# Performance work log

Measured on AMD Instinct MI355X. Metric: run time of the kernel, lower is better.

## Reference

```python
import jax, jax.numpy as jnp
import numpy as np

N_HEAD = 12

def setup_inputs() -> dict:
    key = jax.random.key(0)
    k1, k2, k3 = jax.random.split(key, 3)
    B, T, C = 8, 1024, 768
    x = jax.random.normal(k1, (B, T, C), dtype=jnp.float32)
    # torch Linear(768, 3*768): store as [in, out] so we can do x @ W
    W_attn = jax.random.normal(k2, (C, 3 * C), dtype=jnp.float32) * 0.02
    b_attn = jax.random.normal(k3, (3 * C,), dtype=jnp.float32) * 0.02
    return {"x": x, "W_attn": W_attn, "b_attn": b_attn}

def reference(x, W_attn, b_attn):
    B, T, C = x.shape
    H = N_HEAD
    hs = C // H
    scale = 1.0 / jnp.sqrt(jnp.asarray(hs, dtype=x.dtype))
    qkv = x @ W_attn + b_attn                      # [B,T,3C]
    q, k, v = jnp.split(qkv, 3, axis=-1)
    q = q.reshape(B, T, H, hs).transpose(0, 2, 1, 3)  # [B,H,T,hs]
    k = k.reshape(B, T, H, hs).transpose(0, 2, 1, 3)
    v = v.reshape(B, T, H, hs).transpose(0, 2, 1, 3)
    scores = jnp.einsum('bhqd,bhkd->bhqk', q, k) * scale
    # causal mask then ReLU (masked -inf entries become 0 after ReLU)
    causal = jnp.tril(jnp.ones((T, T), dtype=bool))
    att = jnp.where(causal[None, None], jax.nn.relu(scores), jnp.zeros((), dtype=scores.dtype))
    out = jnp.einsum('bhqk,bhkd->bhqd', att, v)    # [B,H,T,hs]
    out = out.transpose(0, 2, 1, 3).reshape(B, T, C)
    return out
```

## Files before the change

### kernel.cpp

```cpp
#include <hip/hip_runtime.h>

typedef __attribute__((ext_vector_type(8))) short bf16x8;
typedef __attribute__((ext_vector_type(4))) float f32x4;
typedef __attribute__((ext_vector_type(4))) unsigned short us4;
typedef __attribute__((ext_vector_type(8))) unsigned short us8;

#define MFMA(a, b, c) __builtin_amdgcn_mfma_f32_16x16x32_bf16((a), (b), (c), 0, 0, 0)

__device__ __forceinline__ unsigned short f2bf(float f) {
  unsigned u = __builtin_bit_cast(unsigned, f);
  u = (u + 0x7fffu + ((u >> 16) & 1u)) >> 16;
  return (unsigned short)u;
}

__device__ __forceinline__ unsigned cvt_pk_bf16(float lo, float hi) {
  unsigned r;
  asm("v_cvt_pk_bf16_f32 %0, %1, %2" : "=v"(r) : "v"(lo), "v"(hi));
  return r;
}

__device__ __forceinline__ void gload16(const void* g, void* l) {
  __builtin_amdgcn_global_load_lds((const __attribute__((address_space(1))) void*)g,
                                   (__attribute__((address_space(3))) void*)l,
                                   16, 0, 0);
}

__device__ __forceinline__ bf16x8 readfrag(const unsigned short* buf, int row, int kbyte) {
  int byte = row * 128 + kbyte;
  byte ^= (row & 7) << 4;
  return *(const bf16x8*)((const char*)buf + byte);
}

__global__ void cast_x_kernel(const float* __restrict__ x,
                              unsigned short* __restrict__ xb, int n4) {
  int id = blockIdx.x * blockDim.x + threadIdx.x;
  if (id >= n4) return;
  float4 v = ((const float4*)x)[id];
  us4 o = { f2bf(v.x), f2bf(v.y), f2bf(v.z), f2bf(v.w) };
  ((us4*)xb)[id] = o;
}

__global__ void castw_kernel(const float* __restrict__ W,
                             unsigned short* __restrict__ Wt) {
  __shared__ unsigned short tile[32][33];
  int bn = blockIdx.x * 32;
  int bk = blockIdx.y * 32;
  int lx = threadIdx.x & 31, ly = threadIdx.x >> 5;
#pragma unroll
  for (int i = 0; i < 32; i += 8)
    tile[ly + i][lx] = f2bf(W[(bk + ly + i) * 2304 + bn + lx]);
  __syncthreads();
#pragma unroll
  for (int i = 0; i < 32; i += 8)
    Wt[(bn + ly + i) * 768 + bk + lx] = tile[lx][ly + i];
}

__global__ __launch_bounds__(256, 2) void qkv_gemm_kernel(
    const unsigned short* __restrict__ xb, const unsigned short* __restrict__ wt,
    const float* __restrict__ bias,
    unsigned short* __restrict__ qb, unsigned short* __restrict__ kb,
    unsigned short* __restrict__ vb) {
  __shared__ unsigned short lds[40960];
  const int tid = threadIdx.x;
  const int lane = tid & 63, wid = tid >> 6;
  const int wm = wid >> 1, wn = wid & 1;
  const int l15 = lane & 15, lg = lane >> 4;

  int bid = blockIdx.x;
  int xcd = bid & 7, c = bid >> 3;
  int mb = xcd * 8 + (c & 7);
  int nb = c >> 3;
  const int m0 = mb * 128, n0 = nb * 128;

  const unsigned short* Ab_g = xb + (size_t)m0 * 768;
  const unsigned short* Bb_g = wt + (size_t)n0 * 768;

  int eA[4], sA[4];
#pragma unroll
  for (int i = 0; i < 4; ++i) {
    int e = (i * 256 + tid) * 8, row = e >> 6;
    eA[i] = e;
    sA[i] = row * 768 + ((e ^ ((row & 7) << 3)) & 63);
  }

#define SA(buf, k0, i) gload16(Ab_g + sA[i] + (k0), &lds[(buf) * 8192 + eA[i]])
#define SB(buf, k0, i) gload16(Bb_g + sA[i] + (k0), &lds[24576 + (buf) * 8192 + eA[i]])

  f32x4 acc[4][4] = {};
  bf16x8 bfr[4][2];

  SA(0, 0, 0); SA(0, 0, 1); SA(0, 0, 2); SA(0, 0, 3);
  SB(0, 0, 0); SB(0, 0, 1); SB(0, 0, 2); SB(0, 0, 3);
  SA(1, 64, 0); SA(1, 64, 1); SA(1, 64, 2); SA(1, 64, 3);
  asm volatile("s_waitcnt vmcnt(4)" ::: "memory");
  __builtin_amdgcn_s_barrier();

#define GPHASE(cA_, cB_, P, STG, EW)                                              \
  {                                                                               \
    const unsigned short* Abuf = &lds[(cA_) * 8192];                              \
    const unsigned short* Bbuf = &lds[24576 + (cB_) * 8192];                      \
    bf16x8 afr[2][2];                                                             \
    _Pragma("unroll") for (int m2 = 0; m2 < 2; ++m2)                              \
        _Pragma("unroll") for (int kk = 0; kk < 2; ++kk)                          \
            afr[m2][kk] =                                                         \
        readfrag(Abuf, wm * 64 + ((P) * 2 + m2) * 16 + l15, kk * 64 + lg * 16);   \
    if ((P) == 0) {                                                               \
      _Pragma("unroll") for (int nf = 0; nf < 4; ++nf)                            \
          _Pragma("unroll") for (int kk = 0; kk < 2; ++kk)                        \
              bfr[nf][kk] =                                                       \
          readfrag(Bbuf, wn * 64 + nf * 16 + l15, kk * 64 + lg * 16);             \
    }                                                                             \
    STG;                                                                          \
    __builtin_amdgcn_sched_barrier(0);                                            \
    __builtin_amdgcn_s_barrier();                                                 \
    asm volatile("s_waitcnt lgkmcnt(0)" ::: "memory");                            \
    __builtin_amdgcn_sched_barrier(0);                                            \
    __builtin_amdgcn_s_setprio(1);                                                \
    _Pragma("unroll") for (int m2 = 0; m2 < 2; ++m2)                              \
        _Pragma("unroll") for (int nf = 0; nf < 4; ++nf)                          \
            _Pragma("unroll") for (int kk = 0; kk < 2; ++kk)                      \
                acc[(P) * 2 + m2][nf] =                                           \
        MFMA(afr[m2][kk], bfr[nf][kk], acc[(P) * 2 + m2][nf]);                    \
    __builtin_amdgcn_s_setprio(0);                                                \
    EW;                                                                           \
    __builtin_amdgcn_sched_barrier(0);                                            \
    __builtin_amdgcn_s_barrier();                                                 \
  }

  int cA = 0;
  for (int t = 0; t < 10; ++t) {
    int cB = t & 1, cBn = cB ^ 1;
    int cA2 = cA + 2; if (cA2 >= 3) cA2 -= 3;
    int k1 = (t + 1) * 64, k2 = (t + 2) * 64;
    GPHASE(cA, cB, 0, { SB(cBn, k1, 0); SB(cBn, k1, 1); SB(cBn, k1, 2); SB(cBn, k1, 3); }, );
    GPHASE(cA, cB, 1, { SA(cA2, k2, 0); SA(cA2, k2, 1); SA(cA2, k2, 2); SA(cA2, k2, 3); },
           asm volatile("s_waitcnt vmcnt(4)" ::: "memory"));
    cA = (cA == 2) ? 0 : cA + 1;
  }
  GPHASE(cA, 0, 0, { SB(1, 704, 0); SB(1, 704, 1); SB(1, 704, 2); SB(1, 704, 3); }, );
  GPHASE(cA, 0, 1, , asm volatile("s_waitcnt vmcnt(0)" ::: "memory"));
  cA = (cA == 2) ? 0 : cA + 1;
  GPHASE(cA, 1, 0, , );
  GPHASE(cA, 1, 1, , );

  __syncthreads();

  const int sec = n0 / 768;
  const float qs = (sec == 0) ? 0.125f : 1.0f;
  float bcol[4];
#pragma unroll
  for (int nf = 0; nf < 4; ++nf) bcol[nf] = bias[n0 + wn * 64 + nf * 16 + l15];

  if (sec < 2) {
    unsigned short* ct = lds;
#pragma unroll
    for (int mf = 0; mf < 4; ++mf)
#pragma unroll
      for (int nf = 0; nf < 4; ++nf)
#pragma unroll
        for (int r = 0; r < 4; ++r)
          ct[(wm * 64 + mf * 16 + lg * 4 + r) * 128 + wn * 64 + nf * 16 + l15] =
              f2bf((acc[mf][nf][r] + bcol[nf]) * qs);
    __syncthreads();
    unsigned short* dstbase = (sec == 0) ? qb : kb;
    const int hbase = (n0 - sec * 768) >> 6;
    const int g8 = tid >> 3, l8 = tid & 7;
#pragma unroll
    for (int j = 0; j < 8; ++j) {
      int chunk = j * 32 + g8;
      int row = chunk >> 1, hh = chunk & 1;
      us8 v = *(const us8*)&ct[row * 128 + hh * 64 + l8 * 8];
      int t = m0 + row, bb = t >> 10, tt = t & 1023;
      *(us8*)(dstbase + ((size_t)((bb * 12 + hbase + hh) * 1024 + tt)) * 64 + l8 * 8) = v;
    }
  } else {
#pragma unroll
    for (int nf = 0; nf < 4; ++nf) {
      int cc2 = (n0 - 1536) + wn * 64 + nf * 16 + l15;
      int h = cc2 >> 6, d = cc2 & 63;
#pragma unroll
      for (int mf = 0; mf < 4; ++mf) {
        int row0 = m0 + wm * 64 + mf * 16 + lg * 4;
        int bb = row0 >> 10, t0 = row0 & 1023;
        us4 o;
#pragma unroll
        for (int r = 0; r < 4; ++r) o[r] = f2bf(acc[mf][nf][r] + bcol[nf]);
        *(us4*)(vb + ((size_t)((bb * 12 + h) * 64 + d)) * 1024 + t0) = o;
      }
    }
  }
#undef SA
#undef SB
#undef GPHASE
}

__global__ __launch_bounds__(512, 2) void attn_kernel(
    const unsigned short* __restrict__ qb, const unsigned short* __restrict__ kb,
    const unsigned short* __restrict__ vb, float* __restrict__ out) {
  __shared__ unsigned short lds[65536];
  const int tid = threadIdx.x;
  const int lane = tid & 63, wid = tid >> 6;
  const int qs = wid >> 1, ks = wid & 1;
  const int l15 = lane & 15, lg = lane >> 4;

  int bid = blockIdx.x;
  int xcd = bid & 7, c = bid >> 3;
  int bh = xcd * 12 + (c % 12);
  int byq = 3 - (c / 12);
  const int b = bh / 12, h = bh % 12;
  const size_t base = (size_t)bh * 65536;
  const int Q = byq * 4 + qs;
  const int qr0 = byq * 256 + qs * 64;

  bf16x8 aq[4][2];
#pragma unroll
  for (int mf = 0; mf < 4; ++mf)
#pragma unroll
    for (int kk = 0; kk < 2; ++kk)
      aq[mf][kk] = *(const bf16x8*)(qb + base + (size_t)(qr0 + mf * 16 + l15) * 64 +
                                    kk * 32 + lg * 8);

  const int e = tid * 8;
  const int row = e >> 6;
  const int esw = e ^ ((row & 7) << 3);

#define ASTAGE(buf, i_)                                                            \
  {                                                                                \
    int kt0 = 2 * (i_);                                                            \
    gload16(kb + base + (size_t)kt0 * 4096 + esw, &lds[(buf) * 8192 + e]);         \
    gload16(kb + base + (size_t)(kt0 + 1) * 4096 + esw,                            \
            &lds[(buf) * 8192 + 4096 + e]);                                        \
    gload16(vb + base + (size_t)row * 1024 + kt0 * 64 + (esw & 63),                \
            &lds[16384 + (buf) * 8192 + e]);                                       \
    gload16(vb + base + (size_t)row * 1024 + (kt0 + 1) * 64 + (esw & 63),          \
            &lds[16384 + (buf) * 8192 + 4096 + e]);                                \
  }

  f32x4 o[4][4] = {};
  unsigned short* Sb = &lds[32768 + wid * 4096];

  const int niter = 2 * byq + 2;
  ASTAGE(0, 0);
  asm volatile("s_waitcnt vmcnt(0)" ::: "memory");
  __builtin_amdgcn_s_barrier();

  for (int i = 0; i < niter; ++i) {
    const int cur = i & 1;
    if (i + 1 < niter) ASTAGE(cur ^ 1, i + 1);
    const int kt = 2 * i + ks;
    if (kt <= Q) {
      const unsigned short* Kb = &lds[cur * 8192 + ks * 4096];
      const unsigned short* Vb = &lds[16384 + cur * 8192 + ks * 4096];
      bf16x8 bk[4][2];
#pragma unroll
      for (int nf = 0; nf < 4; ++nf)
#pragma unroll
        for (int kk = 0; kk < 2; ++kk)
          bk[nf][kk] = readfrag(Kb, nf * 16 + l15, kk * 64 + lg * 16);
      const bool diag = (kt == Q);
      __builtin_amdgcn_s_setprio(1);
#pragma unroll
      for (int mf = 0; mf < 4; ++mf)
#pragma unroll
        for (int nf = 0; nf < 4; ++nf) {
          f32x4 s = {};
          s = MFMA(bk[nf][0], aq[mf][0], s);
          s = MFMA(bk[nf][1], aq[mf][1], s);
          float v0, v1, v2, v3;
          if (diag) {
            int q = mf * 16 + l15, k0 = nf * 16 + lg * 4;
            v0 = (k0 + 0 <= q) ? fmaxf(s[0], 0.0f) : 0.0f;
            v1 = (k0 + 1 <= q) ? fmaxf(s[1], 0.0f) : 0.0f;
            v2 = (k0 + 2 <= q) ? fmaxf(s[2], 0.0f) : 0.0f;
            v3 = (k0 + 3 <= q) ? fmaxf(s[3], 0.0f) : 0.0f;
          } else {
            v0 = fmaxf(s[0], 0.0f);
            v1 = fmaxf(s[1], 0.0f);
            v2 = fmaxf(s[2], 0.0f);
            v3 = fmaxf(s[3], 0.0f);
          }
          uint2 w;
          w.x = cvt_pk_bf16(v0, v1);
          w.y = cvt_pk_bf16(v2, v3);
          int rowq = mf * 16 + l15;
          int byte = (rowq * 128 + (nf * 16 + lg * 4) * 2) ^ ((rowq & 7) << 4);
          *(uint2*)((char*)Sb + byte) = w;
        }
      __builtin_amdgcn_s_setprio(0);
      bf16x8 pa[4][2];
#pragma unroll
      for (int mf = 0; mf < 4; ++mf)
#pragma unroll
        for (int kk = 0; kk < 2; ++kk)
          pa[mf][kk] = readfrag(Sb, mf * 16 + l15, kk * 64 + lg * 16);
      __builtin_amdgcn_s_setprio(1);
#pragma unroll
      for (int mf = 0; mf < 4; ++mf)
#pragma unroll
        for (int df = 0; df < 4; ++df)
#pragma unroll
          for (int kk = 0; kk < 2; ++kk)
            o[mf][df] = MFMA(pa[mf][kk], readfrag(Vb, df * 16 + l15, kk * 64 + lg * 16),
                             o[mf][df]);
      __builtin_amdgcn_s_setprio(0);
    }
    asm volatile("s_waitcnt vmcnt(0)" ::: "memory");
    __builtin_amdgcn_sched_barrier(0);
    __builtin_amdgcn_s_barrier();
  }
#undef ASTAGE

  float* fr = (float*)lds;
  if (ks == 1) {
#pragma unroll
    for (int mf = 0; mf < 4; ++mf)
#pragma unroll
      for (int df = 0; df < 4; ++df)
#pragma unroll
        for (int r = 0; r < 4; ++r) {
          int rowq = mf * 16 + lg * 4 + r, col = df * 16 + l15;
          int idx = (qs * 4096 + rowq * 64 + col) ^ ((rowq & 4) << 2);
          fr[idx] = o[mf][df][r];
        }
  }
  __syncthreads();
  if (ks == 0) {
#pragma unroll
    for (int mf = 0; mf < 4; ++mf)
#pragma unroll
      for (int df = 0; df < 4; ++df)
#pragma unroll
        for (int r = 0; r < 4; ++r) {
          int rowq = mf * 16 + lg * 4 + r, col = df * 16 + l15;
          int idx = (qs * 4096 + rowq * 64 + col) ^ ((rowq & 4) << 2);
          float v = o[mf][df][r] + fr[idx];
          out[(size_t)(b * 1024 + qr0 + rowq) * 768 + h * 64 + col] = v;
        }
  }
}

extern "C" void kernel_launch(void* const* d_in, const int* in_sizes, int n_in,
                              void* d_out, int out_size, void* d_ws, size_t ws_size,
                              hipStream_t stream) {
  const float* x = (const float*)d_in[0];
  const float* W = (const float*)d_in[1];
  const float* bias = (const float*)d_in[2];
  float* out = (float*)d_out;

  unsigned short* xb = (unsigned short*)d_ws;
  unsigned short* wt = xb + 6291456;
  unsigned short* qb = wt + 1769472;
  unsigned short* kb = qb + 6291456;
  unsigned short* vb = kb + 6291456;

  cast_x_kernel<<<6144, 256, 0, stream>>>(x, xb, 1572864);
  castw_kernel<<<dim3(72, 24), 256, 0, stream>>>(W, wt);
  qkv_gemm_kernel<<<1152, 256, 0, stream>>>(xb, wt, bias, qb, kb, vb);
  attn_kernel<<<384, 512, 0, stream>>>(qb, kb, vb, out);
}
```

Baseline: 84.09 us.

## Keep P in registers via 16x16x16 MFMA and drop key-split waves

New measurement: 86.92 us. 3.4% more time.

```diff
diff --git a/kernel.cpp b/kernel.cpp
--- a/kernel.cpp
+++ b/kernel.cpp
@@ -1,11 +1,13 @@
 #include <hip/hip_runtime.h>
 
 typedef __attribute__((ext_vector_type(8))) short bf16x8;
+typedef __attribute__((ext_vector_type(4))) short bf16x4;
 typedef __attribute__((ext_vector_type(4))) float f32x4;
 typedef __attribute__((ext_vector_type(4))) unsigned short us4;
 typedef __attribute__((ext_vector_type(8))) unsigned short us8;
 
 #define MFMA(a, b, c) __builtin_amdgcn_mfma_f32_16x16x32_bf16((a), (b), (c), 0, 0, 0)
+#define MFMA16(a, b, c) __builtin_amdgcn_mfma_f32_16x16x16bf16_1k((a), (b), (c), 0, 0, 0)
 
 __device__ __forceinline__ unsigned short f2bf(float f) {
   unsigned u = __builtin_bit_cast(unsigned, f);
@@ -29,6 +31,11 @@
   int byte = row * 128 + kbyte;
   byte ^= (row & 7) << 4;
   return *(const bf16x8*)((const char*)buf + byte);
+}
+
+__device__ __forceinline__ bf16x4 readfrag64(const unsigned short* buf, int row, int col) {
+  int byte = (row * 128 + col * 2) ^ ((row & 7) << 4);
+  return *(const bf16x4*)((const char*)buf + byte);
 }
 
 __global__ void cast_x_kernel(const float* __restrict__ x,
@@ -146,7 +153,7 @@
   __syncthreads();
 
   const int sec = n0 / 768;
-  const float qs = (sec == 0) ? 0.125f : 1.0f;
+  const float qscale = (sec == 0) ? 0.125f : 1.0f;
   float bcol[4];
 #pragma unroll
   for (int nf = 0; nf < 4; ++nf) bcol[nf] = bias[n0 + wn * 64 + nf * 16 + l15];
@@ -160,7 +167,7 @@
 #pragma unroll
         for (int r = 0; r < 4; ++r)
           ct[(wm * 64 + mf * 16 + lg * 4 + r) * 128 + wn * 64 + nf * 16 + l15] =
-              f2bf((acc[mf][nf][r] + bcol[nf]) * qs);
+              f2bf((acc[mf][nf][r] + bcol[nf]) * qscale);
     __syncthreads();
     unsigned short* dstbase = (sec == 0) ? qb : kb;
     const int hbase = (n0 - sec * 768) >> 6;
@@ -194,13 +201,12 @@
 #undef GPHASE
 }
 
-__global__ __launch_bounds__(512, 2) void attn_kernel(
+__global__ __launch_bounds__(256, 2) void attn_kernel(
     const unsigned short* __restrict__ qb, const unsigned short* __restrict__ kb,
     const unsigned short* __restrict__ vb, float* __restrict__ out) {
-  __shared__ unsigned short lds[65536];
+  __shared__ unsigned short lds[16384];
   const int tid = threadIdx.x;
   const int lane = tid & 63, wid = tid >> 6;
-  const int qs = wid >> 1, ks = wid & 1;
   const int l15 = lane & 15, lg = lane >> 4;
 
   int bid = blockIdx.x;
@@ -209,8 +215,8 @@
   int byq = 3 - (c / 12);
   const int b = bh / 12, h = bh % 12;
   const size_t base = (size_t)bh * 65536;
-  const int Q = byq * 4 + qs;
-  const int qr0 = byq * 256 + qs * 64;
+  const int Q = byq * 4 + wid;
+  const int qr0 = byq * 256 + wid * 64;
 
   bf16x8 aq[4][2];
 #pragma unroll
@@ -223,41 +229,47 @@
   const int e = tid * 8;
   const int row = e >> 6;
   const int esw = e ^ ((row & 7) << 3);
-
-#define ASTAGE(buf, i_)                                                            \
+  const int e2 = (256 + tid) * 8;
+  const int row2 = e2 >> 6;
+  const int esw2 = e2 ^ ((row2 & 7) << 3);
+
+#define ASTAGE(buf, kt)                                                            \
   {                                                                                \
-    int kt0 = 2 * (i_);                                                            \
-    gload16(kb + base + (size_t)kt0 * 4096 + esw, &lds[(buf) * 8192 + e]);         \
-    gload16(kb + base + (size_t)(kt0 + 1) * 4096 + esw,                            \
-            &lds[(buf) * 8192 + 4096 + e]);                                        \
-    gload16(vb + base + (size_t)row * 1024 + kt0 * 64 + (esw & 63),                \
-            &lds[16384 + (buf) * 8192 + e]);                                       \
-    gload16(vb + base + (size_t)row * 1024 + (kt0 + 1) * 64 + (esw & 63),          \
-            &lds[16384 + (buf) * 8192 + 4096 + e]);                                \
+    gload16(kb + base + (size_t)(kt) * 4096 + esw, &lds[(buf) * 4096 + e]);        \
+    gload16(kb + base + (size_t)(kt) * 4096 + esw2, &lds[(buf) * 4096 + e2]);      \
+    gload16(vb + base + (size_t)row * 1024 + (kt) * 64 + (esw & 63),               \
+            &lds[8192 + (buf) * 4096 + e]);                                        \
+    gload16(vb + base + (size_t)row2 * 1024 + (kt) * 64 + (esw2 & 63),             \
+            &lds[8192 + (buf) * 4096 + e2]);                                       \
   }
 
   f32x4 o[4][4] = {};
-  unsigned short* Sb = &lds[32768 + wid * 4096];
-
-  const int niter = 2 * byq + 2;
+
+  const int NT = byq * 4 + 4;
   ASTAGE(0, 0);
   asm volatile("s_waitcnt vmcnt(0)" ::: "memory");
   __builtin_amdgcn_s_barrier();
 
-  for (int i = 0; i < niter; ++i) {
+  for (int i = 0; i < NT; ++i) {
     const int cur = i & 1;
-    if (i + 1 < niter) ASTAGE(cur ^ 1, i + 1);
-    const int kt = 2 * i + ks;
-    if (kt <= Q) {
-      const unsigned short* Kb = &lds[cur * 8192 + ks * 4096];
-      const unsigned short* Vb = &lds[16384 + cur * 8192 + ks * 4096];
+    if (i + 1 < NT) ASTAGE(cur ^ 1, i + 1);
+    if (i <= Q) {
+      const unsigned short* Kb = &lds[cur * 4096];
+      const unsigned short* Vb = &lds[8192 + cur * 4096];
       bf16x8 bk[4][2];
 #pragma unroll
       for (int nf = 0; nf < 4; ++nf)
 #pragma unroll
         for (int kk = 0; kk < 2; ++kk)
           bk[nf][kk] = readfrag(Kb, nf * 16 + l15, kk * 64 + lg * 16);
-      const bool diag = (kt == Q);
+      bf16x4 vf[4][4];
+#pragma unroll
+      for (int nf = 0; nf < 4; ++nf)
+#pragma unroll
+        for (int df = 0; df < 4; ++df)
+          vf[nf][df] = readfrag64(Vb, df * 16 + l15, nf * 16 + lg * 4);
+      const bool diag = (i == Q);
+      bf16x4 pa[4][4];
       __builtin_amdgcn_s_setprio(1);
 #pragma unroll
       for (int mf = 0; mf < 4; ++mf)
@@ -282,26 +294,15 @@
           uint2 w;
           w.x = cvt_pk_bf16(v0, v1);
           w.y = cvt_pk_bf16(v2, v3);
-          int rowq = mf * 16 + l15;
-          int byte = (rowq * 128 + (nf * 16 + lg * 4) * 2) ^ ((rowq & 7) << 4);
-          *(uint2*)((char*)Sb + byte) = w;
+          pa[mf][nf] = __builtin_bit_cast(bf16x4, w);
         }
-      __builtin_amdgcn_s_setprio(0);
-      bf16x8 pa[4][2];
-#pragma unroll
-      for (int mf = 0; mf < 4; ++mf)
-#pragma unroll
-        for (int kk = 0; kk < 2; ++kk)
-          pa[mf][kk] = readfrag(Sb, mf * 16 + l15, kk * 64 + lg * 16);
-      __builtin_amdgcn_s_setprio(1);
-#pragma unroll
-      for (int mf = 0; mf < 4; ++mf)
-#pragma unroll
-        for (int df = 0; df < 4; ++df)
-#pragma unroll
-          for (int kk = 0; kk < 2; ++kk)
-            o[mf][df] = MFMA(pa[mf][kk], readfrag(Vb, df * 16 + l15, kk * 64 + lg * 16),
-                             o[mf][df]);
+#pragma unroll
+      for (int nf = 0; nf < 4; ++nf)
+#pragma unroll
+        for (int mf = 0; mf < 4; ++mf)
+#pragma unroll
+          for (int df = 0; df < 4; ++df)
+            o[mf][df] = MFMA16(pa[mf][nf], vf[nf][df], o[mf][df]);
       __builtin_amdgcn_s_setprio(0);
     }
     asm volatile("s_waitcnt vmcnt(0)" ::: "memory");
@@ -310,33 +311,15 @@
   }
 #undef ASTAGE
 
-  float* fr = (float*)lds;
-  if (ks == 1) {
-#pragma unroll
-    for (int mf = 0; mf < 4; ++mf)
-#pragma unroll
-      for (int df = 0; df < 4; ++df)
-#pragma unroll
-        for (int r = 0; r < 4; ++r) {
-          int rowq = mf * 16 + lg * 4 + r, col = df * 16 + l15;
-          int idx = (qs * 4096 + rowq * 64 + col) ^ ((rowq & 4) << 2);
-          fr[idx] = o[mf][df][r];
-        }
-  }
-  __syncthreads();
-  if (ks == 0) {
-#pragma unroll
-    for (int mf = 0; mf < 4; ++mf)
-#pragma unroll
-      for (int df = 0; df < 4; ++df)
-#pragma unroll
-        for (int r = 0; r < 4; ++r) {
-          int rowq = mf * 16 + lg * 4 + r, col = df * 16 + l15;
-          int idx = (qs * 4096 + rowq * 64 + col) ^ ((rowq & 4) << 2);
-          float v = o[mf][df][r] + fr[idx];
-          out[(size_t)(b * 1024 + qr0 + rowq) * 768 + h * 64 + col] = v;
-        }
-  }
+#pragma unroll
+  for (int mf = 0; mf < 4; ++mf)
+#pragma unroll
+    for (int df = 0; df < 4; ++df)
+#pragma unroll
+      for (int r = 0; r < 4; ++r) {
+        int rowq = mf * 16 + lg * 4 + r, col = df * 16 + l15;
+        out[(size_t)(b * 1024 + qr0 + rowq) * 768 + h * 64 + col] = o[mf][df][r];
+      }
 }
 
 extern "C" void kernel_launch(void* const* d_in, const int* in_sizes, int n_in,
@@ -356,5 +339,5 @@
   cast_x_kernel<<<6144, 256, 0, stream>>>(x, xb, 1572864);
   castw_kernel<<<dim3(72, 24), 256, 0, stream>>>(W, wt);
   qkv_gemm_kernel<<<1152, 256, 0, stream>>>(xb, wt, bias, qb, kb, vb);
-  attn_kernel<<<384, 512, 0, stream>>>(qb, kb, vb, out);
-}
+  attn_kernel<<<384, 256, 0, stream>>>(qb, kb, vb, out);
+}
```

## Keep attention probabilities in registers and use 16x16x16 MFMA for PV

Applied to the files above, without the earlier changes.

Result: no change. 84.63 us (+0.6%).

```diff
diff --git a/kernel.cpp b/kernel.cpp
--- a/kernel.cpp
+++ b/kernel.cpp
@@ -1,11 +1,13 @@
 #include <hip/hip_runtime.h>
 
 typedef __attribute__((ext_vector_type(8))) short bf16x8;
+typedef __attribute__((ext_vector_type(4))) short bf16x4;
 typedef __attribute__((ext_vector_type(4))) float f32x4;
 typedef __attribute__((ext_vector_type(4))) unsigned short us4;
 typedef __attribute__((ext_vector_type(8))) unsigned short us8;
 
 #define MFMA(a, b, c) __builtin_amdgcn_mfma_f32_16x16x32_bf16((a), (b), (c), 0, 0, 0)
+#define MFMA16(a, b, c) __builtin_amdgcn_mfma_f32_16x16x16bf16_1k((a), (b), (c), 0, 0, 0)
 
 __device__ __forceinline__ unsigned short f2bf(float f) {
   unsigned u = __builtin_bit_cast(unsigned, f);
@@ -29,6 +31,11 @@
   int byte = row * 128 + kbyte;
   byte ^= (row & 7) << 4;
   return *(const bf16x8*)((const char*)buf + byte);
+}
+
+__device__ __forceinline__ bf16x4 readfrag64(const unsigned short* buf, int row, int col) {
+  int byte = (row * 128 + col * 2) ^ ((row & 7) << 4);
+  return *(const bf16x4*)((const char*)buf + byte);
 }
 
 __global__ void cast_x_kernel(const float* __restrict__ x,
@@ -146,7 +153,7 @@
   __syncthreads();
 
   const int sec = n0 / 768;
-  const float qs = (sec == 0) ? 0.125f : 1.0f;
+  const float qscale = (sec == 0) ? 0.125f : 1.0f;
   float bcol[4];
 #pragma unroll
   for (int nf = 0; nf < 4; ++nf) bcol[nf] = bias[n0 + wn * 64 + nf * 16 + l15];
@@ -160,7 +167,7 @@
 #pragma unroll
         for (int r = 0; r < 4; ++r)
           ct[(wm * 64 + mf * 16 + lg * 4 + r) * 128 + wn * 64 + nf * 16 + l15] =
-              f2bf((acc[mf][nf][r] + bcol[nf]) * qs);
+              f2bf((acc[mf][nf][r] + bcol[nf]) * qscale);
     __syncthreads();
     unsigned short* dstbase = (sec == 0) ? qb : kb;
     const int hbase = (n0 - sec * 768) >> 6;
@@ -197,7 +204,7 @@
 __global__ __launch_bounds__(512, 2) void attn_kernel(
     const unsigned short* __restrict__ qb, const unsigned short* __restrict__ kb,
     const unsigned short* __restrict__ vb, float* __restrict__ out) {
-  __shared__ unsigned short lds[65536];
+  __shared__ unsigned short lds[32768];
   const int tid = threadIdx.x;
   const int lane = tid & 63, wid = tid >> 6;
   const int qs = wid >> 1, ks = wid & 1;
@@ -237,7 +244,6 @@
   }
 
   f32x4 o[4][4] = {};
-  unsigned short* Sb = &lds[32768 + wid * 4096];
 
   const int niter = 2 * byq + 2;
   ASTAGE(0, 0);
@@ -257,7 +263,14 @@
 #pragma unroll
         for (int kk = 0; kk < 2; ++kk)
           bk[nf][kk] = readfrag(Kb, nf * 16 + l15, kk * 64 + lg * 16);
+      bf16x4 vf[4][4];
+#pragma unroll
+      for (int nf = 0; nf < 4; ++nf)
+#pragma unroll
+        for (int df = 0; df < 4; ++df)
+          vf[nf][df] = readfrag64(Vb, df * 16 + l15, nf * 16 + lg * 4);
       const bool diag = (kt == Q);
+      bf16x4 pa[4][4];
       __builtin_amdgcn_s_setprio(1);
 #pragma unroll
       for (int mf = 0; mf < 4; ++mf)
@@ -282,26 +295,15 @@
           uint2 w;
           w.x = cvt_pk_bf16(v0, v1);
           w.y = cvt_pk_bf16(v2, v3);
-          int rowq = mf * 16 + l15;
-          int byte = (rowq * 128 + (nf * 16 + lg * 4) * 2) ^ ((rowq & 7) << 4);
-          *(uint2*)((char*)Sb + byte) = w;
+          pa[mf][nf] = __builtin_bit_cast(bf16x4, w);
         }
-      __builtin_amdgcn_s_setprio(0);
-      bf16x8 pa[4][2];
-#pragma unroll
-      for (int mf = 0; mf < 4; ++mf)
-#pragma unroll
-        for (int kk = 0; kk < 2; ++kk)
-          pa[mf][kk] = readfrag(Sb, mf * 16 + l15, kk * 64 + lg * 16);
-      __builtin_amdgcn_s_setprio(1);
-#pragma unroll
-      for (int mf = 0; mf < 4; ++mf)
-#pragma unroll
-        for (int df = 0; df < 4; ++df)
-#pragma unroll
-          for (int kk = 0; kk < 2; ++kk)
-            o[mf][df] = MFMA(pa[mf][kk], readfrag(Vb, df * 16 + l15, kk * 64 + lg * 16),
-                             o[mf][df]);
+#pragma unroll
+      for (int nf = 0; nf < 4; ++nf)
+#pragma unroll
+        for (int mf = 0; mf < 4; ++mf)
+#pragma unroll
+          for (int df = 0; df < 4; ++df)
+            o[mf][df] = MFMA16(pa[mf][nf], vf[nf][df], o[mf][df]);
       __builtin_amdgcn_s_setprio(0);
     }
     asm volatile("s_waitcnt vmcnt(0)" ::: "memory");
```
